# Kernel optimization log

Hardware: AMD Instinct MI355X
Metric: run time of the kernel (lower is better)

## Reference

```python
import jax, jax.numpy as jnp
import numpy as np

ALPHA = 1.702
LIMIT = 7.0
BLOCK = 32  # mxfp4 block size (values per scale)

# fp4 e2m1 lookup table, indexed by 4-bit code (sign in high bit)
FP4_LUT = jnp.array([0.0, 0.5, 1.0, 1.5, 2.0, 3.0, 4.0, 6.0,
                     -0.0, -0.5, -1.0, -1.5, -2.0, -3.0, -4.0, -6.0],
                    dtype=jnp.float32)


def dequant_mxfp4(blocks, scales):
    # blocks: [E, R, C//2] int byte values (two fp4 nibbles per byte, low nibble first)
    # scales: [E, R, C//32] e8m0 exponents; value = 2^(scale - 127)
    E, R, _ = blocks.shape
    nb = scales.shape[-1]
    lo = blocks & 0xF
    hi = (blocks >> 4) & 0xF
    vals = jnp.stack([FP4_LUT[lo], FP4_LUT[hi]], axis=-1)  # [E,R,C//2,2]
    vals = vals.reshape(E, R, nb, BLOCK)
    scale = jnp.exp2((scales - 127).astype(jnp.float32))   # [E,R,nb]
    return (vals * scale[..., None]).reshape(E, R, nb * BLOCK)  # [E,R,C]


def setup_inputs() -> dict:
    key = jax.random.key(0)
    ks = jax.random.split(key, 12)
    T, E, H, I = 1024, 8, 1024, 1024
    inp = {
        'hidden_states': jax.random.normal(ks[0], (T, H), dtype=jnp.float32),
        'router_logits': jax.random.normal(ks[1], (T, E), dtype=jnp.float32),
        'gate_proj_blocks': jax.random.randint(ks[2], (E, I, H // 2), 0, 256, dtype=jnp.int32),
        'gate_proj_scales': jax.random.randint(ks[3], (E, I, H // BLOCK), 121, 130, dtype=jnp.int32),
        'gate_proj_bias': jax.random.normal(ks[4], (E, I), dtype=jnp.float32) * 0.02,
        'up_proj_blocks': jax.random.randint(ks[5], (E, I, H // 2), 0, 256, dtype=jnp.int32),
        'up_proj_scales': jax.random.randint(ks[6], (E, I, H // BLOCK), 121, 130, dtype=jnp.int32),
        'up_proj_bias': jax.random.normal(ks[7], (E, I), dtype=jnp.float32) * 0.02,
        'down_proj_blocks': jax.random.randint(ks[8], (E, H, I // 2), 0, 256, dtype=jnp.int32),
        'down_proj_scales': jax.random.randint(ks[9], (E, H, I // BLOCK), 121, 130, dtype=jnp.int32),
        'down_proj_bias': jax.random.normal(ks[10], (E, H), dtype=jnp.float32) * 0.02,
        'k': 2,
    }
    return inp


def reference(hidden_states, router_logits, gate_proj_blocks, gate_proj_scales,
              gate_proj_bias, up_proj_blocks, up_proj_scales, up_proj_bias,
              down_proj_blocks, down_proj_scales, down_proj_bias, k):
    T, H = hidden_states.shape
    E = router_logits.shape[-1]
    # --- top-k routing: softmax over the selected logits, scattered to [T,E] ---
    top_vals, top_idx = jax.lax.top_k(router_logits, k)        # [T,k]
    top_w = jax.nn.softmax(top_vals, axis=-1)                   # [T,k]
    route = jnp.zeros((T, E), dtype=hidden_states.dtype)
    route = route.at[jnp.arange(T)[:, None], top_idx].add(top_w)  # [T,E]
    # --- dequantize mxfp4 expert weights ---
    gate_w = dequant_mxfp4(gate_proj_blocks, gate_proj_scales)  # [E,I,H]
    up_w = dequant_mxfp4(up_proj_blocks, up_proj_scales)        # [E,I,H]
    down_w = dequant_mxfp4(down_proj_blocks, down_proj_scales)  # [E,H,I]
    # --- GLU expert FFN (GPT-OSS variant) ---
    gate = jnp.einsum('th,eih->tei', hidden_states, gate_w) + gate_proj_bias[None]
    up = jnp.einsum('th,eih->tei', hidden_states, up_w) + up_proj_bias[None]
    gate = jnp.minimum(gate, LIMIT)
    up = jnp.clip(up, -LIMIT, LIMIT)
    glu = gate * jax.nn.sigmoid(gate * ALPHA)
    act = (up + 1.0) * glu                                       # [T,E,I]
    # fold routing weight in before the down projection, then sum over experts
    act = act * route[:, :, None]
    out = jnp.einsum('tei,ehi->th', act, down_w) + route @ down_proj_bias  # [T,H]
    return out
```

## Files before the change

### kernel.cpp

```cpp
#include <hip/hip_runtime.h>
#include <cstdint>
#include <cstddef>

typedef __bf16 bf16x8 __attribute__((ext_vector_type(8)));
typedef float f32x4 __attribute__((ext_vector_type(4)));
typedef unsigned short u16x2 __attribute__((ext_vector_type(2)));

constexpr int HH = 1024;
constexpr int II = 1024;
constexpr int KMAX = 2;
constexpr int EMAX = 8;
constexpr int GU_TILES = 24;
constexpr int DN_TILES = 40;
constexpr float FALPHA = 1.702f;
constexpr float FLIMIT = 7.0f;

__device__ __forceinline__ unsigned pk_add16(unsigned a, unsigned b) {
  u16x2 x, y;
  __builtin_memcpy(&x, &a, 4); __builtin_memcpy(&y, &b, 4);
  u16x2 r = x + y;
  unsigned o; __builtin_memcpy(&o, &r, 4); return o;
}

__device__ __forceinline__ int4 decode_chunk(int4 raw, unsigned addk) {
  unsigned p = (unsigned)raw.x | ((unsigned)raw.y << 8) |
               ((unsigned)raw.z << 16) | ((unsigned)raw.w << 24);
  unsigned q = p >> 4;
  unsigned me = p & 0x07070707u, mo = q & 0x07070707u;
  unsigned se = p & 0x08080808u, so = q & 0x08080808u;
  unsigned hiE = __builtin_amdgcn_perm(0x40404040u, 0x3F3F3F14u, me) | (se << 4);
  unsigned hiO = __builtin_amdgcn_perm(0x40404040u, 0x3F3F3F14u, mo) | (so << 4);
  unsigned loE = __builtin_amdgcn_perm(0xC0804000u, 0xC0800000u, me);
  unsigned loO = __builtin_amdgcn_perm(0xC0804000u, 0xC0800000u, mo);
  int4 out;
  out.x = (int)pk_add16(__builtin_amdgcn_perm(hiE, loE, 0x05010400u), addk);
  out.y = (int)pk_add16(__builtin_amdgcn_perm(hiE, loE, 0x07030602u), addk);
  out.z = (int)pk_add16(__builtin_amdgcn_perm(hiO, loO, 0x05010400u), addk);
  out.w = (int)pk_add16(__builtin_amdgcn_perm(hiO, loO, 0x07030602u), addk);
  return out;
}

__device__ __forceinline__ unsigned make_addk(int s) {
  int k = s - 127;
  unsigned t = ((unsigned)(k << 7)) & 0xFFFFu;
  return t | (t << 16);
}

__device__ __forceinline__ void gll16(const void* g, void* l) {
  __builtin_amdgcn_global_load_lds(
      (const __attribute__((address_space(1))) void*)g,
      (__attribute__((address_space(3))) void*)l, 16, 0, 0);
}

__global__ void routing_kernel(const float* __restrict__ logits, const int* __restrict__ dk,
                               int T, int E, float* __restrict__ route,
                               int* __restrict__ tidx, float* __restrict__ tw) {
  int t = blockIdx.x * blockDim.x + threadIdx.x;
  if (t >= T) return;
  int kk = *dk; if (kk > KMAX) kk = KMAX; if (kk < 1) kk = 1;
  int EE = E > EMAX ? EMAX : E;
  float v[EMAX]; bool used[EMAX];
  for (int e = 0; e < EE; ++e) { v[e] = logits[t * E + e]; used[e] = false; route[t * E + e] = 0.f; }
  float tv[KMAX]; int ti[KMAX];
  for (int j = 0; j < kk; ++j) {
    float best = -3.4e38f; int bi = 0;
    for (int e = 0; e < EE; ++e) if (!used[e] && v[e] > best) { best = v[e]; bi = e; }
    used[bi] = true; tv[j] = best; ti[j] = bi;
  }
  float mx = tv[0], ssum = 0.f, wj[KMAX];
  for (int j = 0; j < kk; ++j) { wj[j] = __expf(tv[j] - mx); ssum += wj[j]; }
  for (int j = 0; j < kk; ++j) {
    float wv = wj[j] / ssum;
    route[t * E + ti[j]] = wv;
    tidx[t * kk + j] = ti[j];
    tw[t * kk + j] = wv;
  }
}

__global__ void build_lists(const int* __restrict__ tidx, const int* __restrict__ dk,
                            int T, int* __restrict__ lists, int* __restrict__ counts) {
  int e = blockIdx.x;
  int lane = threadIdx.x;
  int kk = *dk; if (kk > KMAX) kk = KMAX; if (kk < 1) kk = 1;
  int cnt = 0;
  for (int base = 0; base < T; base += 64) {
    int t = base + lane;
    int j = -1;
    if (t < T) {
      for (int q = 0; q < kk; ++q) if (tidx[t * kk + q] == e) j = q;
    }
    unsigned long long m = __ballot(j >= 0);
    if (j >= 0) {
      int pre = __popcll(m & ((1ull << lane) - 1ull));
      lists[e * T + cnt + pre] = (t << 3) | j;
    }
    cnt += __popcll(m);
  }
  if (lane == 0) counts[e] = cnt;
}

__global__ void build_tiles(const int* __restrict__ counts, int E,
                            int* __restrict__ tabGU, int* __restrict__ tabDN) {
  if (threadIdx.x == 0 && blockIdx.x == 0) {
    int g = 0, d = 0;
    for (int e = 0; e < E && e < EMAX; ++e) {
      int c = counts[e];
      for (int m = 0; m * 128 < c && g < GU_TILES; ++m) tabGU[g++] = (e << 16) | m;
      for (int m = 0; m * 64 < c && d < DN_TILES; ++m) tabDN[d++] = (e << 16) | m;
    }
    for (; g < GU_TILES; ++g) tabGU[g] = -1;
    for (; d < DN_TILES; ++d) tabDN[d] = -1;
  }
}

__global__ void convert_hs(const float* __restrict__ hs, __bf16* __restrict__ hsb, int n8) {
  int g = blockIdx.x * 256 + threadIdx.x;
  if (g >= n8) return;
  const float4* p = (const float4*)hs + (size_t)g * 2;
  float4 a = p[0], b = p[1];
  bf16x8 r;
  r[0] = (__bf16)a.x; r[1] = (__bf16)a.z; r[2] = (__bf16)b.x; r[3] = (__bf16)b.z;
  r[4] = (__bf16)a.y; r[5] = (__bf16)a.w; r[6] = (__bf16)b.y; r[7] = (__bf16)b.w;
  *(bf16x8*)(hsb + (size_t)g * 8) = r;
}

__global__ __launch_bounds__(256, 2) void gemm_gate_up(
    const __bf16* __restrict__ hsb,
    const int* __restrict__ gblk, const int* __restrict__ gscl, const float* __restrict__ gbias,
    const int* __restrict__ ublk, const int* __restrict__ uscl, const float* __restrict__ ubias,
    const int* __restrict__ lists, const int* __restrict__ counts,
    const float* __restrict__ tw, const int* __restrict__ dk,
    const int* __restrict__ tab,
    __bf16* __restrict__ act, int T)
{
  int te = tab[blockIdx.x];
  if (te < 0) return;
  int e = te >> 16, mtile = te & 0xFFFF;
  int cnt = counts[e];
  int n_valid = cnt - mtile * 128;
  if (n_valid <= 0) return;
  if (n_valid > 128) n_valid = 128;
  int kk = *dk; if (kk > KMAX) kk = KMAX; if (kk < 1) kk = 1;

  __shared__ int s_tok[128];
  __shared__ char Abuf[2][16384];
  __shared__ char Bbuf[2][16384];

  int tid = threadIdx.x;
  if (tid < 128) {
    int idx = mtile * 128 + tid;
    s_tok[tid] = lists[e * T + (idx < cnt ? idx : mtile * 128)];
  }
  __syncthreads();

  int lane = tid & 63, w = tid >> 6;
  int r15 = lane & 15, sw = lane & 7;
  int wr = w >> 1, wc = w & 1;

  int cA = (lane & 7) ^ (lane >> 3);
  size_t aOff[4];
  #pragma unroll
  for (int q = 0; q < 4; ++q) {
    int row = w * 32 + q * 8 + (lane >> 3);
    int tok = s_tok[row] >> 3;
    aOff[q] = (size_t)tok * (HH * 2) + (size_t)cA * 16;
  }

  int rB = tid >> 1, c4 = (tid & 1) * 4;
  int gu = (rB >> 4) & 1;
  int iLoc = (rB & 15) | ((rB >> 5) << 4);
  int ibase = blockIdx.y * 64;
  int i_row = ibase + iLoc;
  const int* blk = gu ? ublk : gblk;
  const int* scl = gu ? uscl : gscl;
  const int4* bp = (const int4*)(blk + ((size_t)e * II + i_row) * (HH / 2));
  const int* sp = scl + ((size_t)e * II + i_row) * (HH / 32);

  f32x4 acc[4][4];
  #pragma unroll
  for (int a = 0; a < 4; ++a)
    #pragma unroll
    for (int b = 0; b < 4; ++b) acc[a][b] = (f32x4)0.f;

  #pragma unroll
  for (int q = 0; q < 4; ++q)
    gll16((const char*)hsb + aOff[q], Abuf[0] + w * 4096 + q * 1024);
  {
    int4 rw[4];
    #pragma unroll
    for (int j = 0; j < 4; ++j) rw[j] = bp[c4 + j];
    unsigned addk = make_addk(sp[tid & 1]);
    #pragma unroll
    for (int j = 0; j < 4; ++j)
      *(int4*)(Bbuf[0] + (c4 + j) * 2048 + rB * 16) = decode_chunk(rw[j], addk);
  }
  __syncthreads();

  constexpr int NK = HH / 64;
  for (int kt = 0; kt < NK; ++kt) {
    char* An = Abuf[(kt + 1) & 1];
    char* Bn = Bbuf[(kt + 1) & 1];
    const char* Ac = Abuf[kt & 1];
    const char* Bc = Bbuf[kt & 1];
    int4 rw[4]; unsigned addk = 0;
    if (kt < NK - 1) {
      #pragma unroll
      for (int q = 0; q < 4; ++q)
        gll16((const char*)hsb + aOff[q] + (kt + 1) * 128, An + w * 4096 + q * 1024);
      #pragma unroll
      for (int j = 0; j < 4; ++j) rw[j] = bp[(kt + 1) * 8 + c4 + j];
      addk = make_addk(sp[(kt + 1) * 2 + (tid & 1)]);
    }
    #pragma unroll
    for (int kq = 0; kq < 2; ++kq) {
      int kc = kq * 4 + (lane >> 4);
      bf16x8 bf[4];
      #pragma unroll
      for (int fn = 0; fn < 4; ++fn)
        bf[fn] = *(const bf16x8*)(Bc + kc * 2048 + (wc * 64 + fn * 16 + r15) * 16);
      #pragma unroll
      for (int fm = 0; fm < 4; ++fm) {
        int m = wr * 64 + fm * 16 + r15;
        bf16x8 af = *(const bf16x8*)(Ac + m * 128 + ((kc ^ sw) * 16));
        #pragma unroll
        for (int fn = 0; fn < 4; ++fn)
          acc[fm][fn] = __builtin_amdgcn_mfma_f32_16x16x32_bf16(af, bf[fn], acc[fm][fn], 0, 0, 0);
      }
    }
    if (kt < NK - 1) {
      #pragma unroll
      for (int j = 0; j < 4; ++j)
        *(int4*)(Bn + (c4 + j) * 2048 + rB * 16) = decode_chunk(rw[j], addk);
    }
    __syncthreads();
  }

  #pragma unroll
  for (int fp = 0; fp < 2; ++fp) {
    int i_log = ibase + wc * 32 + fp * 16 + r15;
    float gb = gbias[e * II + i_log], ub = ubias[e * II + i_log];
    int i_phys = (i_log & ~7) | ((r15 & 1) << 2) | ((r15 & 7) >> 1);
    #pragma unroll
    for (int fm = 0; fm < 4; ++fm) {
      #pragma unroll
      for (int rg = 0; rg < 4; ++rg) {
        int mloc = wr * 64 + fm * 16 + (lane >> 4) * 4 + rg;
        if (mloc < n_valid) {
          int entry = s_tok[mloc];
          int t = entry >> 3, j = entry & 7;
          float wv = tw[t * kk + j];
          float g = fminf(acc[fm][fp * 2][rg] + gb, FLIMIT);
          float u = fminf(fmaxf(acc[fm][fp * 2 + 1][rg] + ub, -FLIMIT), FLIMIT);
          float glu = g / (1.f + __expf(-FALPHA * g));
          act[((size_t)t * kk + j) * II + i_phys] = (__bf16)((u + 1.f) * glu * wv);
        }
      }
    }
  }
}

__global__ __launch_bounds__(256, 2) void gemm_down(
    const __bf16* __restrict__ act,
    const int* __restrict__ dblk, const int* __restrict__ dscl,
    const int* __restrict__ lists, const int* __restrict__ counts,
    const int* __restrict__ dk, const int* __restrict__ tab,
    float* __restrict__ partial, int T)
{
  int te = tab[blockIdx.x];
  if (te < 0) return;
  int e = te >> 16, mtile = te & 0xFFFF;
  int cnt = counts[e];
  int n_valid = cnt - mtile * 64;
  if (n_valid <= 0) return;
  if (n_valid > 64) n_valid = 64;
  int kk = *dk; if (kk > KMAX) kk = KMAX; if (kk < 1) kk = 1;

  __shared__ int s_tok[64];
  __shared__ char Abuf[2][8192];
  __shared__ char Bbuf[2][16384];

  int tid = threadIdx.x;
  if (tid < 64) {
    int idx = mtile * 64 + tid;
    s_tok[tid] = lists[e * T + (idx < cnt ? idx : mtile * 64)];
  }
  __syncthreads();

  int lane = tid & 63, w = tid >> 6;
  int r15 = lane & 15, sw = lane & 7;
  int wr = w >> 1, wc = w & 1;

  int cA = (lane & 7) ^ (lane >> 3);
  size_t aOff[2];
  #pragma unroll
  for (int q = 0; q < 2; ++q) {
    int row = w * 16 + q * 8 + (lane >> 3);
    int entry = s_tok[row];
    size_t slot = (size_t)(entry >> 3) * kk + (entry & 7);
    aOff[q] = slot * (II * 2) + (size_t)cA * 16;
  }

  int rB = tid >> 1, c4 = (tid & 1) * 4;
  int hbase = blockIdx.y * 128;
  int h_row = hbase + rB;
  const int4* bp = (const int4*)(dblk + ((size_t)e * HH + h_row) * (II / 2));
  const int* sp = dscl + ((size_t)e * HH + h_row) * (II / 32);

  f32x4 acc[2][4];
  #pragma unroll
  for (int a = 0; a < 2; ++a)
    #pragma unroll
    for (int b = 0; b < 4; ++b) acc[a][b] = (f32x4)0.f;

  #pragma unroll
  for (int q = 0; q < 2; ++q)
    gll16((const char*)act + aOff[q], Abuf[0] + w * 2048 + q * 1024);
  {
    int4 rw[4];
    #pragma unroll
    for (int j = 0; j < 4; ++j) rw[j] = bp[c4 + j];
    unsigned addk = make_addk(sp[tid & 1]);
    #pragma unroll
    for (int j = 0; j < 4; ++j)
      *(int4*)(Bbuf[0] + (c4 + j) * 2048 + rB * 16) = decode_chunk(rw[j], addk);
  }
  __syncthreads();

  constexpr int NK = II / 64;
  for (int kt = 0; kt < NK; ++kt) {
    char* An = Abuf[(kt + 1) & 1];
    char* Bn = Bbuf[(kt + 1) & 1];
    const char* Ac = Abuf[kt & 1];
    const char* Bc = Bbuf[kt & 1];
    int4 rw[4]; unsigned addk = 0;
    if (kt < NK - 1) {
      #pragma unroll
      for (int q = 0; q < 2; ++q)
        gll16((const char*)act + aOff[q] + (kt + 1) * 128, An + w * 2048 + q * 1024);
      #pragma unroll
      for (int j = 0; j < 4; ++j) rw[j] = bp[(kt + 1) * 8 + c4 + j];
      addk = make_addk(sp[(kt + 1) * 2 + (tid & 1)]);
    }
    #pragma unroll
    for (int kq = 0; kq < 2; ++kq) {
      int kc = kq * 4 + (lane >> 4);
      bf16x8 bf[4];
      #pragma unroll
      for (int fn = 0; fn < 4; ++fn)
        bf[fn] = *(const bf16x8*)(Bc + kc * 2048 + (wc * 64 + fn * 16 + r15) * 16);
      #pragma unroll
      for (int fm = 0; fm < 2; ++fm) {
        int m = wr * 32 + fm * 16 + r15;
        bf16x8 af = *(const bf16x8*)(Ac + m * 128 + ((kc ^ sw) * 16));
        #pragma unroll
        for (int fn = 0; fn < 4; ++fn)
          acc[fm][fn] = __builtin_amdgcn_mfma_f32_16x16x32_bf16(af, bf[fn], acc[fm][fn], 0, 0, 0);
      }
    }
    if (kt < NK - 1) {
      #pragma unroll
      for (int j = 0; j < 4; ++j)
        *(int4*)(Bn + (c4 + j) * 2048 + rB * 16) = decode_chunk(rw[j], addk);
    }
    __syncthreads();
  }

  #pragma unroll
  for (int fm = 0; fm < 2; ++fm) {
    #pragma unroll
    for (int rg = 0; rg < 4; ++rg) {
      int mloc = wr * 32 + fm * 16 + (lane >> 4) * 4 + rg;
      if (mloc < n_valid) {
        int entry = s_tok[mloc];
        int t = entry >> 3, j = entry & 7;
        size_t slot = (size_t)t * kk + j;
        #pragma unroll
        for (int fn = 0; fn < 4; ++fn) {
          int h = hbase + wc * 64 + fn * 16 + r15;
          partial[slot * HH + h] = acc[fm][fn][rg];
        }
      }
    }
  }
}

__global__ void combine_kernel(const float* __restrict__ partial, const float* __restrict__ route,
                               const float* __restrict__ dbias, const int* __restrict__ dk,
                               float* __restrict__ out, int E) {
  int t = blockIdx.y;
  int h = blockIdx.x * 256 + threadIdx.x;
  int kk = *dk; if (kk > KMAX) kk = KMAX; if (kk < 1) kk = 1;
  float s = 0.f;
  for (int j = 0; j < kk; ++j) s += partial[((size_t)t * kk + j) * HH + h];
  for (int e = 0; e < E; ++e) s += route[t * E + e] * dbias[(size_t)e * HH + h];
  out[(size_t)t * HH + h] = s;
}

extern "C" void kernel_launch(void* const* d_in, const int* in_sizes, int n_in,
                              void* d_out, int out_size, void* d_ws, size_t ws_size,
                              hipStream_t stream) {
  const float* hs    = (const float*)d_in[0];
  const float* rl    = (const float*)d_in[1];
  const int*   gblk  = (const int*)d_in[2];
  const int*   gscl  = (const int*)d_in[3];
  const float* gbias = (const float*)d_in[4];
  const int*   ublk  = (const int*)d_in[5];
  const int*   uscl  = (const int*)d_in[6];
  const float* ubias = (const float*)d_in[7];
  const int*   dblk  = (const int*)d_in[8];
  const int*   dscl  = (const int*)d_in[9];
  const float* dbias = (const float*)d_in[10];
  const int*   dk    = (const int*)d_in[11];

  long s0 = in_sizes[0], s1 = in_sizes[1], s2 = in_sizes[2], s4 = in_sizes[4];
  int H = (int)(2 * s2 / s4);
  int T = (int)(s0 / H);
  int E = (int)(s1 / T);

  char* w = (char*)d_ws;
  auto alloc = [&](size_t bytes) { char* p = w; w += (bytes + 255) & ~size_t(255); return p; };
  float*  route   = (float*)alloc(sizeof(float) * (size_t)T * E);
  int*    tidx    = (int*)  alloc(sizeof(int)   * (size_t)T * KMAX);
  float*  twp     = (float*)alloc(sizeof(float) * (size_t)T * KMAX);
  int*    counts  = (int*)  alloc(sizeof(int)   * (size_t)E);
  int*    lists   = (int*)  alloc(sizeof(int)   * (size_t)E * T);
  int*    tabGU   = (int*)  alloc(sizeof(int)   * GU_TILES);
  int*    tabDN   = (int*)  alloc(sizeof(int)   * DN_TILES);
  __bf16* hsb     = (__bf16*)alloc(sizeof(__bf16) * (size_t)T * HH);
  __bf16* act     = (__bf16*)alloc(sizeof(__bf16) * (size_t)T * KMAX * II);
  float*  partial = (float*)alloc(sizeof(float) * (size_t)T * KMAX * HH);

  routing_kernel<<<dim3((T + 255) / 256), 256, 0, stream>>>(rl, dk, T, E, route, tidx, twp);
  build_lists<<<dim3(E), 64, 0, stream>>>(tidx, dk, T, lists, counts);
  build_tiles<<<dim3(1), 64, 0, stream>>>(counts, E, tabGU, tabDN);
  convert_hs<<<dim3((T * HH / 8 + 255) / 256), 256, 0, stream>>>(hs, hsb, T * HH / 8);
  gemm_gate_up<<<dim3(GU_TILES, II * 2 / 128), 256, 0, stream>>>(
      hsb, gblk, gscl, gbias, ublk, uscl, ubias, lists, counts, twp, dk, tabGU, act, T);
  gemm_down<<<dim3(DN_TILES, HH / 128), 256, 0, stream>>>(
      act, dblk, dscl, lists, counts, dk, tabDN, partial, T);
  combine_kernel<<<dim3(HH / 256, T), 256, 0, stream>>>(partial, route, dbias, dk, (float*)d_out, E);
}
```

Baseline: 106.7 us.

## Decode mxfp4 weights into registers with hardware cvt and drop LDS B staging

Both GEMMs now have each lane load and decode its own MFMA B fragment directly into registers, using the gfx950 scaled fp4-to-bf16 convert builtin when available, replacing the LDS B double buffer and its shared-memory writes and reads. The gate/up kernel moves to 512 threads with smaller per-wave M tiles. The down-projection partial output is stored as bf16 instead of fp32 to halve combine traffic. B weights are no longer shared across waves in the block, so each wave re-fetches them from global/L2. The bf16 partials also lose some precision.

Result: slower. 207.2 us (+94.1%).

```diff
diff --git a/kernel.cpp b/kernel.cpp
--- a/kernel.cpp
+++ b/kernel.cpp
@@ -3,6 +3,7 @@
 #include <cstddef>
 
 typedef __bf16 bf16x8 __attribute__((ext_vector_type(8)));
+typedef __bf16 bf16x2 __attribute__((ext_vector_type(2)));
 typedef float f32x4 __attribute__((ext_vector_type(4)));
 typedef unsigned short u16x2 __attribute__((ext_vector_type(2)));
 
@@ -15,13 +16,18 @@
 constexpr float FALPHA = 1.702f;
 constexpr float FLIMIT = 7.0f;
 
+#if __has_builtin(__builtin_amdgcn_cvt_scalef32_pk_bf16_fp4)
+#define USE_CVT 1
+#else
+#define USE_CVT 0
+#endif
+
 __device__ __forceinline__ unsigned pk_add16(unsigned a, unsigned b) {
   u16x2 x, y;
   __builtin_memcpy(&x, &a, 4); __builtin_memcpy(&y, &b, 4);
   u16x2 r = x + y;
   unsigned o; __builtin_memcpy(&o, &r, 4); return o;
 }
-
 __device__ __forceinline__ int4 decode_chunk(int4 raw, unsigned addk) {
   unsigned p = (unsigned)raw.x | ((unsigned)raw.y << 8) |
                ((unsigned)raw.z << 16) | ((unsigned)raw.w << 24);
@@ -39,11 +45,30 @@
   out.w = (int)pk_add16(__builtin_amdgcn_perm(hiO, loO, 0x07030602u), addk);
   return out;
 }
-
 __device__ __forceinline__ unsigned make_addk(int s) {
   int k = s - 127;
   unsigned t = ((unsigned)(k << 7)) & 0xFFFFu;
   return t | (t << 16);
+}
+
+__device__ __forceinline__ bf16x8 decode_frag(int4 raw, int s) {
+#if USE_CVT
+  unsigned t0 = __builtin_amdgcn_perm((unsigned)raw.y, (unsigned)raw.x, 0x00000400u);
+  unsigned t1 = __builtin_amdgcn_perm((unsigned)raw.w, (unsigned)raw.z, 0x00000400u);
+  unsigned p  = __builtin_amdgcn_perm(t1, t0, 0x05040100u);
+  float scf = __uint_as_float((unsigned)s << 23);
+  bf16x2 a = __builtin_amdgcn_cvt_scalef32_pk_bf16_fp4(p, scf, 0);
+  bf16x2 b = __builtin_amdgcn_cvt_scalef32_pk_bf16_fp4(p, scf, 1);
+  bf16x2 c = __builtin_amdgcn_cvt_scalef32_pk_bf16_fp4(p, scf, 2);
+  bf16x2 d = __builtin_amdgcn_cvt_scalef32_pk_bf16_fp4(p, scf, 3);
+  bf16x8 r;
+  r[0]=a[0]; r[1]=a[1]; r[2]=b[0]; r[3]=b[1]; r[4]=c[0]; r[5]=c[1]; r[6]=d[0]; r[7]=d[1];
+  return r;
+#else
+  int4 d4 = decode_chunk(raw, make_addk(s));
+  bf16x8 r; __builtin_memcpy(&r, &d4, 16);
+  return r;
+#endif
 }
 
 __device__ __forceinline__ void gll16(const void* g, void* l) {
@@ -119,12 +144,17 @@
   const float4* p = (const float4*)hs + (size_t)g * 2;
   float4 a = p[0], b = p[1];
   bf16x8 r;
+#if USE_CVT
+  r[0] = (__bf16)a.x; r[1] = (__bf16)a.y; r[2] = (__bf16)a.z; r[3] = (__bf16)a.w;
+  r[4] = (__bf16)b.x; r[5] = (__bf16)b.y; r[6] = (__bf16)b.z; r[7] = (__bf16)b.w;
+#else
   r[0] = (__bf16)a.x; r[1] = (__bf16)a.z; r[2] = (__bf16)b.x; r[3] = (__bf16)b.z;
   r[4] = (__bf16)a.y; r[5] = (__bf16)a.w; r[6] = (__bf16)b.y; r[7] = (__bf16)b.w;
+#endif
   *(bf16x8*)(hsb + (size_t)g * 8) = r;
 }
 
-__global__ __launch_bounds__(256, 2) void gemm_gate_up(
+__global__ __launch_bounds__(512, 2) void gemm_gate_up(
     const __bf16* __restrict__ hsb,
     const int* __restrict__ gblk, const int* __restrict__ gscl, const float* __restrict__ gbias,
     const int* __restrict__ ublk, const int* __restrict__ uscl, const float* __restrict__ ubias,
@@ -144,7 +174,6 @@
 
   __shared__ int s_tok[128];
   __shared__ char Abuf[2][16384];
-  __shared__ char Bbuf[2][16384];
 
   int tid = threadIdx.x;
   if (tid < 128) {
@@ -154,83 +183,90 @@
   __syncthreads();
 
   int lane = tid & 63, w = tid >> 6;
-  int r15 = lane & 15, sw = lane & 7;
+  int r15 = lane & 15, kg = lane >> 4;
   int wr = w >> 1, wc = w & 1;
 
   int cA = (lane & 7) ^ (lane >> 3);
-  size_t aOff[4];
-  #pragma unroll
-  for (int q = 0; q < 4; ++q) {
-    int row = w * 32 + q * 8 + (lane >> 3);
+  unsigned aOff[2];
+  #pragma unroll
+  for (int q = 0; q < 2; ++q) {
+    int row = w * 16 + q * 8 + (lane >> 3);
     int tok = s_tok[row] >> 3;
-    aOff[q] = (size_t)tok * (HH * 2) + (size_t)cA * 16;
-  }
-
-  int rB = tid >> 1, c4 = (tid & 1) * 4;
-  int gu = (rB >> 4) & 1;
-  int iLoc = (rB & 15) | ((rB >> 5) << 4);
+    aOff[q] = (unsigned)tok * (HH * 2) + (unsigned)cA * 16;
+  }
+
   int ibase = blockIdx.y * 64;
-  int i_row = ibase + iLoc;
-  const int* blk = gu ? ublk : gblk;
-  const int* scl = gu ? uscl : gscl;
-  const int4* bp = (const int4*)(blk + ((size_t)e * II + i_row) * (HH / 2));
-  const int* sp = scl + ((size_t)e * II + i_row) * (HH / 32);
-
-  f32x4 acc[4][4];
-  #pragma unroll
-  for (int a = 0; a < 4; ++a)
+  const int4* bp[4]; const int* sp[4];
+  #pragma unroll
+  for (int fn = 0; fn < 4; ++fn) {
+    int i_g = ibase + wc * 32 + (fn >> 1) * 16 + r15;
+    const int* blkb = (fn & 1) ? ublk : gblk;
+    const int* sclb = (fn & 1) ? uscl : gscl;
+    bp[fn] = (const int4*)(blkb + ((size_t)e * II + i_g) * (HH / 2));
+    sp[fn] = sclb + ((size_t)e * II + i_g) * (HH / 32);
+  }
+
+  f32x4 acc[2][4];
+  #pragma unroll
+  for (int a = 0; a < 2; ++a)
     #pragma unroll
     for (int b = 0; b < 4; ++b) acc[a][b] = (f32x4)0.f;
 
-  #pragma unroll
-  for (int q = 0; q < 4; ++q)
-    gll16((const char*)hsb + aOff[q], Abuf[0] + w * 4096 + q * 1024);
-  {
-    int4 rw[4];
-    #pragma unroll
-    for (int j = 0; j < 4; ++j) rw[j] = bp[c4 + j];
-    unsigned addk = make_addk(sp[tid & 1]);
-    #pragma unroll
-    for (int j = 0; j < 4; ++j)
-      *(int4*)(Bbuf[0] + (c4 + j) * 2048 + rB * 16) = decode_chunk(rw[j], addk);
+  bf16x8 bcur[4][2];
+  int4 rw[4][2];
+  int2 sc4[4];
+
+  #pragma unroll
+  for (int q = 0; q < 2; ++q)
+    gll16((const char*)hsb + aOff[q], Abuf[0] + (w * 16 + q * 8) * 128 + lane * 16);
+  #pragma unroll
+  for (int fn = 0; fn < 4; ++fn) {
+    #pragma unroll
+    for (int kq = 0; kq < 2; ++kq) rw[fn][kq] = bp[fn][kq * 4 + kg];
+    sc4[fn] = *(const int2*)(sp[fn]);
   }
   __syncthreads();
+  #pragma unroll
+  for (int fn = 0; fn < 4; ++fn) {
+    bcur[fn][0] = decode_frag(rw[fn][0], sc4[fn].x);
+    bcur[fn][1] = decode_frag(rw[fn][1], sc4[fn].y);
+  }
 
   constexpr int NK = HH / 64;
+  #pragma unroll 1
   for (int kt = 0; kt < NK; ++kt) {
+    const char* Ac = Abuf[kt & 1];
     char* An = Abuf[(kt + 1) & 1];
-    char* Bn = Bbuf[(kt + 1) & 1];
-    const char* Ac = Abuf[kt & 1];
-    const char* Bc = Bbuf[kt & 1];
-    int4 rw[4]; unsigned addk = 0;
-    if (kt < NK - 1) {
-      #pragma unroll
-      for (int q = 0; q < 4; ++q)
-        gll16((const char*)hsb + aOff[q] + (kt + 1) * 128, An + w * 4096 + q * 1024);
-      #pragma unroll
-      for (int j = 0; j < 4; ++j) rw[j] = bp[(kt + 1) * 8 + c4 + j];
-      addk = make_addk(sp[(kt + 1) * 2 + (tid & 1)]);
+    if (kt + 1 < NK) {
+      #pragma unroll
+      for (int q = 0; q < 2; ++q)
+        gll16((const char*)hsb + aOff[q] + (kt + 1) * 128,
+              An + (w * 16 + q * 8) * 128 + lane * 16);
+      #pragma unroll
+      for (int fn = 0; fn < 4; ++fn) {
+        #pragma unroll
+        for (int kq = 0; kq < 2; ++kq) rw[fn][kq] = bp[fn][(kt + 1) * 8 + kq * 4 + kg];
+        sc4[fn] = *(const int2*)(sp[fn] + (kt + 1) * 2);
+      }
     }
     #pragma unroll
     for (int kq = 0; kq < 2; ++kq) {
-      int kc = kq * 4 + (lane >> 4);
-      bf16x8 bf[4];
-      #pragma unroll
-      for (int fn = 0; fn < 4; ++fn)
-        bf[fn] = *(const bf16x8*)(Bc + kc * 2048 + (wc * 64 + fn * 16 + r15) * 16);
-      #pragma unroll
-      for (int fm = 0; fm < 4; ++fm) {
-        int m = wr * 64 + fm * 16 + r15;
-        bf16x8 af = *(const bf16x8*)(Ac + m * 128 + ((kc ^ sw) * 16));
+      int kc = kq * 4 + kg;
+      #pragma unroll
+      for (int fm = 0; fm < 2; ++fm) {
+        int m = wr * 32 + fm * 16 + r15;
+        bf16x8 af = *(const bf16x8*)(Ac + m * 128 + ((kc ^ (m & 7)) * 16));
         #pragma unroll
         for (int fn = 0; fn < 4; ++fn)
-          acc[fm][fn] = __builtin_amdgcn_mfma_f32_16x16x32_bf16(af, bf[fn], acc[fm][fn], 0, 0, 0);
-      }
-    }
-    if (kt < NK - 1) {
-      #pragma unroll
-      for (int j = 0; j < 4; ++j)
-        *(int4*)(Bn + (c4 + j) * 2048 + rB * 16) = decode_chunk(rw[j], addk);
+          acc[fm][fn] = __builtin_amdgcn_mfma_f32_16x16x32_bf16(af, bcur[fn][kq], acc[fm][fn], 0, 0, 0);
+      }
+    }
+    if (kt + 1 < NK) {
+      #pragma unroll
+      for (int fn = 0; fn < 4; ++fn) {
+        bcur[fn][0] = decode_frag(rw[fn][0], sc4[fn].x);
+        bcur[fn][1] = decode_frag(rw[fn][1], sc4[fn].y);
+      }
     }
     __syncthreads();
   }
@@ -239,12 +275,16 @@
   for (int fp = 0; fp < 2; ++fp) {
     int i_log = ibase + wc * 32 + fp * 16 + r15;
     float gb = gbias[e * II + i_log], ub = ubias[e * II + i_log];
-    int i_phys = (i_log & ~7) | ((r15 & 1) << 2) | ((r15 & 7) >> 1);
-    #pragma unroll
-    for (int fm = 0; fm < 4; ++fm) {
+#if USE_CVT
+    int i_st = i_log;
+#else
+    int i_st = (i_log & ~7) | ((i_log & 1) << 2) | ((i_log & 7) >> 1);
+#endif
+    #pragma unroll
+    for (int fm = 0; fm < 2; ++fm) {
       #pragma unroll
       for (int rg = 0; rg < 4; ++rg) {
-        int mloc = wr * 64 + fm * 16 + (lane >> 4) * 4 + rg;
+        int mloc = wr * 32 + fm * 16 + kg * 4 + rg;
         if (mloc < n_valid) {
           int entry = s_tok[mloc];
           int t = entry >> 3, j = entry & 7;
@@ -252,7 +292,7 @@
           float g = fminf(acc[fm][fp * 2][rg] + gb, FLIMIT);
           float u = fminf(fmaxf(acc[fm][fp * 2 + 1][rg] + ub, -FLIMIT), FLIMIT);
           float glu = g / (1.f + __expf(-FALPHA * g));
-          act[((size_t)t * kk + j) * II + i_phys] = (__bf16)((u + 1.f) * glu * wv);
+          act[((size_t)t * kk + j) * II + i_st] = (__bf16)((u + 1.f) * glu * wv);
         }
       }
     }
@@ -264,7 +304,7 @@
     const int* __restrict__ dblk, const int* __restrict__ dscl,
     const int* __restrict__ lists, const int* __restrict__ counts,
     const int* __restrict__ dk, const int* __restrict__ tab,
-    float* __restrict__ partial, int T)
+    __bf16* __restrict__ partial, int T)
 {
   int te = tab[blockIdx.x];
   if (te < 0) return;
@@ -277,7 +317,6 @@
 
   __shared__ int s_tok[64];
   __shared__ char Abuf[2][8192];
-  __shared__ char Bbuf[2][16384];
 
   int tid = threadIdx.x;
   if (tid < 64) {
@@ -287,24 +326,27 @@
   __syncthreads();
 
   int lane = tid & 63, w = tid >> 6;
-  int r15 = lane & 15, sw = lane & 7;
+  int r15 = lane & 15, kg = lane >> 4;
   int wr = w >> 1, wc = w & 1;
 
   int cA = (lane & 7) ^ (lane >> 3);
-  size_t aOff[2];
+  unsigned aOff[2];
   #pragma unroll
   for (int q = 0; q < 2; ++q) {
     int row = w * 16 + q * 8 + (lane >> 3);
     int entry = s_tok[row];
-    size_t slot = (size_t)(entry >> 3) * kk + (entry & 7);
-    aOff[q] = slot * (II * 2) + (size_t)cA * 16;
-  }
-
-  int rB = tid >> 1, c4 = (tid & 1) * 4;
+    unsigned slot = (unsigned)(entry >> 3) * kk + (entry & 7);
+    aOff[q] = slot * (II * 2) + (unsigned)cA * 16;
+  }
+
   int hbase = blockIdx.y * 128;
-  int h_row = hbase + rB;
-  const int4* bp = (const int4*)(dblk + ((size_t)e * HH + h_row) * (II / 2));
-  const int* sp = dscl + ((size_t)e * HH + h_row) * (II / 32);
+  const int4* bp[4]; const int* sp[4];
+  #pragma unroll
+  for (int fn = 0; fn < 4; ++fn) {
+    int h = hbase + wc * 64 + fn * 16 + r15;
+    bp[fn] = (const int4*)(dblk + ((size_t)e * HH + h) * (II / 2));
+    sp[fn] = dscl + ((size_t)e * HH + h) * (II / 32);
+  }
 
   f32x4 acc[2][4];
   #pragma unroll
@@ -312,55 +354,61 @@
     #pragma unroll
     for (int b = 0; b < 4; ++b) acc[a][b] = (f32x4)0.f;
 
+  bf16x8 bcur[4][2];
+  int4 rw[4][2];
+  int2 sc4[4];
+
   #pragma unroll
   for (int q = 0; q < 2; ++q)
-    gll16((const char*)act + aOff[q], Abuf[0] + w * 2048 + q * 1024);
-  {
-    int4 rw[4];
-    #pragma unroll
-    for (int j = 0; j < 4; ++j) rw[j] = bp[c4 + j];
-    unsigned addk = make_addk(sp[tid & 1]);
-    #pragma unroll
-    for (int j = 0; j < 4; ++j)
-      *(int4*)(Bbuf[0] + (c4 + j) * 2048 + rB * 16) = decode_chunk(rw[j], addk);
+    gll16((const char*)act + aOff[q], Abuf[0] + (w * 16 + q * 8) * 128 + lane * 16);
+  #pragma unroll
+  for (int fn = 0; fn < 4; ++fn) {
+    #pragma unroll
+    for (int kq = 0; kq < 2; ++kq) rw[fn][kq] = bp[fn][kq * 4 + kg];
+    sc4[fn] = *(const int2*)(sp[fn]);
   }
   __syncthreads();
+  #pragma unroll
+  for (int fn = 0; fn < 4; ++fn) {
+    bcur[fn][0] = decode_frag(rw[fn][0], sc4[fn].x);
+    bcur[fn][1] = decode_frag(rw[fn][1], sc4[fn].y);
+  }
 
   constexpr int NK = II / 64;
+  #pragma unroll 1
   for (int kt = 0; kt < NK; ++kt) {
+    const char* Ac = Abuf[kt & 1];
     char* An = Abuf[(kt + 1) & 1];
-    char* Bn = Bbuf[(kt + 1) & 1];
-    const char* Ac = Abuf[kt & 1];
-    const char* Bc = Bbuf[kt & 1];
-    int4 rw[4]; unsigned addk = 0;
-    if (kt < NK - 1) {
+    if (kt + 1 < NK) {
       #pragma unroll
       for (int q = 0; q < 2; ++q)
-        gll16((const char*)act + aOff[q] + (kt + 1) * 128, An + w * 2048 + q * 1024);
-      #pragma unroll
-      for (int j = 0; j < 4; ++j) rw[j] = bp[(kt + 1) * 8 + c4 + j];
-      addk = make_addk(sp[(kt + 1) * 2 + (tid & 1)]);
+        gll16((const char*)act + aOff[q] + (kt + 1) * 128,
+              An + (w * 16 + q * 8) * 128 + lane * 16);
+      #pragma unroll
+      for (int fn = 0; fn < 4; ++fn) {
+        #pragma unroll
+        for (int kq = 0; kq < 2; ++kq) rw[fn][kq] = bp[fn][(kt + 1) * 8 + kq * 4 + kg];
+        sc4[fn] = *(const int2*)(sp[fn] + (kt + 1) * 2);
+      }
     }
     #pragma unroll
     for (int kq = 0; kq < 2; ++kq) {
-      int kc = kq * 4 + (lane >> 4);
-      bf16x8 bf[4];
-      #pragma unroll
-      for (int fn = 0; fn < 4; ++fn)
-        bf[fn] = *(const bf16x8*)(Bc + kc * 2048 + (wc * 64 + fn * 16 + r15) * 16);
+      int kc = kq * 4 + kg;
       #pragma unroll
       for (int fm = 0; fm < 2; ++fm) {
         int m = wr * 32 + fm * 16 + r15;
-        bf16x8 af = *(const bf16x8*)(Ac + m * 128 + ((kc ^ sw) * 16));
+        bf16x8 af = *(const bf16x8*)(Ac + m * 128 + ((kc ^ (m & 7)) * 16));
         #pragma unroll
         for (int fn = 0; fn < 4; ++fn)
-          acc[fm][fn] = __builtin_amdgcn_mfma_f32_16x16x32_bf16(af, bf[fn], acc[fm][fn], 0, 0, 0);
-      }
-    }
-    if (kt < NK - 1) {
-      #pragma unroll
-      for (int j = 0; j < 4; ++j)
-        *(int4*)(Bn + (c4 + j) * 2048 + rB * 16) = decode_chunk(rw[j], addk);
+          acc[fm][fn] = __builtin_amdgcn_mfma_f32_16x16x32_bf16(af, bcur[fn][kq], acc[fm][fn], 0, 0, 0);
+      }
+    }
+    if (kt + 1 < NK) {
+      #pragma unroll
+      for (int fn = 0; fn < 4; ++fn) {
+        bcur[fn][0] = decode_frag(rw[fn][0], sc4[fn].x);
+        bcur[fn][1] = decode_frag(rw[fn][1], sc4[fn].y);
+      }
     }
     __syncthreads();
   }
@@ -369,7 +417,7 @@
   for (int fm = 0; fm < 2; ++fm) {
     #pragma unroll
     for (int rg = 0; rg < 4; ++rg) {
-      int mloc = wr * 32 + fm * 16 + (lane >> 4) * 4 + rg;
+      int mloc = wr * 32 + fm * 16 + kg * 4 + rg;
       if (mloc < n_valid) {
         int entry = s_tok[mloc];
         int t = entry >> 3, j = entry & 7;
@@ -377,21 +425,21 @@
         #pragma unroll
         for (int fn = 0; fn < 4; ++fn) {
           int h = hbase + wc * 64 + fn * 16 + r15;
-          partial[slot * HH + h] = acc[fm][fn][rg];
+          partial[slot * HH + h] = (__bf16)acc[fm][fn][rg];
         }
       }
     }
   }
 }
 
-__global__ void combine_kernel(const float* __restrict__ partial, const float* __restrict__ route,
+__global__ void combine_kernel(const __bf16* __restrict__ partial, const float* __restrict__ route,
                                const float* __restrict__ dbias, const int* __restrict__ dk,
                                float* __restrict__ out, int E) {
   int t = blockIdx.y;
   int h = blockIdx.x * 256 + threadIdx.x;
   int kk = *dk; if (kk > KMAX) kk = KMAX; if (kk < 1) kk = 1;
   float s = 0.f;
-  for (int j = 0; j < kk; ++j) s += partial[((size_t)t * kk + j) * HH + h];
+  for (int j = 0; j < kk; ++j) s += (float)partial[((size_t)t * kk + j) * HH + h];
   for (int e = 0; e < E; ++e) s += route[t * E + e] * dbias[(size_t)e * HH + h];
   out[(size_t)t * HH + h] = s;
 }
@@ -428,13 +476,13 @@
   int*    tabDN   = (int*)  alloc(sizeof(int)   * DN_TILES);
   __bf16* hsb     = (__bf16*)alloc(sizeof(__bf16) * (size_t)T * HH);
   __bf16* act     = (__bf16*)alloc(sizeof(__bf16) * (size_t)T * KMAX * II);
-  float*  partial = (float*)alloc(sizeof(float) * (size_t)T * KMAX * HH);
+  __bf16* partial = (__bf16*)alloc(sizeof(__bf16) * (size_t)T * KMAX * HH);
 
   routing_kernel<<<dim3((T + 255) / 256), 256, 0, stream>>>(rl, dk, T, E, route, tidx, twp);
   build_lists<<<dim3(E), 64, 0, stream>>>(tidx, dk, T, lists, counts);
   build_tiles<<<dim3(1), 64, 0, stream>>>(counts, E, tabGU, tabDN);
   convert_hs<<<dim3((T * HH / 8 + 255) / 256), 256, 0, stream>>>(hs, hsb, T * HH / 8);
-  gemm_gate_up<<<dim3(GU_TILES, II * 2 / 128), 256, 0, stream>>>(
+  gemm_gate_up<<<dim3(GU_TILES, II / 64), 512, 0, stream>>>(
       hsb, gblk, gscl, gbias, ublk, uscl, ubias, lists, counts, twp, dk, tabGU, act, T);
   gemm_down<<<dim3(DN_TILES, HH / 128), 256, 0, stream>>>(
       act, dblk, dscl, lists, counts, dk, tabDN, partial, T);
```
